# Kernel tuning notes

Hardware: AMD Instinct MI355X
Metric: run time of the kernel (lower is better)

The kernel has to match this reference:

```python
import jax, jax.numpy as jnp
import numpy as np

N, E = 100000, 1200000
IN_DIM, HID, OUT = 128, 64, 64
EPS = 1e-5


def _glorot(key, shape):
    lim = 1.0 / np.sqrt(shape[0])
    return jax.random.uniform(key, shape, jnp.float32, -lim, lim)


def setup_inputs() -> dict:
    key = jax.random.key(0)
    ks = jax.random.split(key, 20)
    inp = {
        'x': jax.random.normal(ks[0], (N, IN_DIM), jnp.float32),
        'edge_index': jax.random.randint(ks[1], (2, E), 0, N, jnp.int64),
        'xgb_scores': jax.random.uniform(ks[2], (N,), jnp.float32),
        # SAGEConv params: W_l (aggregated path, with bias), W_r (root path, no bias)
        'W1l': _glorot(ks[3], (IN_DIM, HID)), 'b1': jnp.zeros((HID,), jnp.float32), 'W1r': _glorot(ks[4], (IN_DIM, HID)),
        'g1': jnp.ones((HID,), jnp.float32), 'be1': jnp.zeros((HID,), jnp.float32),
        'W2l': _glorot(ks[5], (HID, HID)), 'b2': jnp.zeros((HID,), jnp.float32), 'W2r': _glorot(ks[6], (HID, HID)),
        'g2': jnp.ones((HID,), jnp.float32), 'be2': jnp.zeros((HID,), jnp.float32),
        'W3l': _glorot(ks[7], (HID, OUT)), 'b3': jnp.zeros((OUT,), jnp.float32), 'W3r': _glorot(ks[8], (HID, OUT)),
        'g3': jnp.ones((OUT,), jnp.float32), 'be3': jnp.zeros((OUT,), jnp.float32),
        # fusion MLP: Linear(out+1, 64) -> ReLU -> Linear(64, 1)
        'Wf1': _glorot(ks[9], (OUT + 1, 64)), 'bf1': jnp.zeros((64,), jnp.float32),
        'Wf2': _glorot(ks[10], (64, 1)), 'bf2': jnp.zeros((1,), jnp.float32),
    }
    return inp


def _sage_conv(x, src, dst, Wl, b, Wr, n):
    # mean aggregation of source features at destination nodes (PyG SAGEConv, aggr='mean')
    agg = jax.ops.segment_sum(x[src], dst, num_segments=n)           # (N, d)
    cnt = jax.ops.segment_sum(jnp.ones((src.shape[0],), x.dtype), dst, num_segments=n)
    mean = agg / jnp.clip(cnt, 1.0)[:, None]
    return mean @ Wl + b + x @ Wr


def _bn(h, g, b):
    mu = jnp.mean(h, axis=0)
    var = jnp.var(h, axis=0)  # biased, as in torch BN training normalization
    return (h - mu) * jax.lax.rsqrt(var + EPS) * g + b


def reference(x, edge_index, xgb_scores,
              W1l, b1, W1r, g1, be1,
              W2l, b2, W2r, g2, be2,
              W3l, b3, W3r, g3, be3,
              Wf1, bf1, Wf2, bf2):
    n = x.shape[0]
    src, dst = edge_index[0], edge_index[1]
    # dropout is identity in eval; BN uses batch statistics
    h = jax.nn.relu(_bn(_sage_conv(x, src, dst, W1l, b1, W1r, n), g1, be1))
    h = jax.nn.relu(_bn(_sage_conv(h, src, dst, W2l, b2, W2r, n), g2, be2))
    h = jax.nn.relu(_bn(_sage_conv(h, src, dst, W3l, b3, W3r, n), g3, be3))
    combined = jnp.concatenate([h, xgb_scores[:, None]], axis=1)     # (N, out+1)
    z = jax.nn.relu(combined @ Wf1 + bf1)
    logits = (z @ Wf2 + bf2)[:, 0]
    return logits
```

## Files before the change

### kernel.cpp

```cpp
#include <hip/hip_runtime.h>


typedef __attribute__((ext_vector_type(8))) short bf16x8;
typedef __attribute__((ext_vector_type(4))) float f32x4;

#define ELLS 48

__device__ __forceinline__ ushort f2bf(float f) {
  unsigned u = __float_as_uint(f);
  return (ushort)((u + 0x7fff + ((u >> 16) & 1)) >> 16);
}
__device__ __forceinline__ float bf2f(ushort h) {
  return __uint_as_float((unsigned)h << 16);
}
__device__ __forceinline__ void unpack8(uint4 v, float* f) {
  f[0] = __uint_as_float(v.x << 16);
  f[1] = __uint_as_float(v.x & 0xffff0000u);
  f[2] = __uint_as_float(v.y << 16);
  f[3] = __uint_as_float(v.y & 0xffff0000u);
  f[4] = __uint_as_float(v.z << 16);
  f[5] = __uint_as_float(v.z & 0xffff0000u);
  f[6] = __uint_as_float(v.w << 16);
  f[7] = __uint_as_float(v.w & 0xffff0000u);
}


__device__ __forceinline__ void prep_one(const float* __restrict__ Wl,
                                         const float* __restrict__ Wr,
                                         ushort* __restrict__ Whi,
                                         ushort* __restrict__ Wlo, int din,
                                         int i) {
  int col = i / din, k = i % din;
  float v = (col < 64) ? Wl[(size_t)k * 64 + col]
                       : Wr[(size_t)k * 64 + (col - 64)];
  ushort h = f2bf(v);
  Whi[i] = h;
  Wlo[i] = f2bf(v - bf2f(h));
}

__global__ __launch_bounds__(256) void prep_all(
    const float* __restrict__ W1l, const float* __restrict__ W1r,
    ushort* __restrict__ Whi1, ushort* __restrict__ Wlo1,
    const float* __restrict__ W2l, const float* __restrict__ W2r,
    ushort* __restrict__ Whi2, ushort* __restrict__ Wlo2,
    const float* __restrict__ W3l, const float* __restrict__ W3r,
    ushort* __restrict__ Whi3, ushort* __restrict__ Wlo3,
    int* __restrict__ deg, float* __restrict__ stats,
    ushort* __restrict__ sent, int n, int nbd) {
  int bid = blockIdx.x;
  const int tid = threadIdx.x;
  if (bid < nbd) {
    int i = bid * 256 + tid;
    if (i < n + 4) deg[i] = 0;
    return;
  }
  bid -= nbd;
  if (bid < 64) {
    prep_one(W1l, W1r, Whi1, Wlo1, 128, bid * 256 + tid);
    return;
  }
  bid -= 64;
  if (bid < 32) {
    prep_one(W2l, W2r, Whi2, Wlo2, 64, bid * 256 + tid);
    return;
  }
  bid -= 32;
  if (bid < 32) {
    prep_one(W3l, W3r, Whi3, Wlo3, 64, bid * 256 + tid);
    return;
  }
  if (tid < 384) stats[tid] = 0.f;
  if (tid < 64) sent[tid] = 0;
}


__global__ __launch_bounds__(256) void ell_fill_sharded(
    const int* __restrict__ ei, int* __restrict__ deg, int* __restrict__ ell,
    int E, int n, int bps) {
  const int shard = blockIdx.x / bps;
  const int bib = blockIdx.x % bps;
  const int chunk = n >> 3;
  const int lo = shard * chunk;
  const int hi = (shard == 7) ? n : lo + chunk;
  for (int e = bib * 256 + threadIdx.x; e < E; e += bps * 256) {
    int d = __builtin_nontemporal_load(ei + E + e);
    if (d >= lo && d < hi) {
      int s = __builtin_nontemporal_load(ei + e);
      int pos = atomicAdd(&deg[d], 1);
      if (pos < ELLS) ell[(size_t)d * ELLS + pos] = s;
    }
  }
}

template <int DIN, bool NORM, bool XBF16>
__global__ __launch_bounds__(256) void gemm_mfma(
    const void* __restrict__ Xv, const float* __restrict__ stats,
    const float* __restrict__ g, const float* __restrict__ be,
    const float* __restrict__ bias, const ushort* __restrict__ Whi,
    const ushort* __restrict__ Wlo, ushort* __restrict__ Ybf,
    ushort* __restrict__ Yrbf, int n) {
  constexpr int WS = 40;
  __shared__ ushort sW[2 * 128 * WS];
  __shared__ float sSS[128];
  __shared__ float sB[64];
  const int tid = threadIdx.x;
  const int w = tid >> 6;
  const int lane = tid & 63;
  const int m = lane & 15;
  const int quad = lane >> 4;
  const int row0 = blockIdx.x * 64;

  if (tid < 64) {
    sB[tid] = bias[tid];
    if (NORM) {
      float invn = 1.0f / (float)n;
      float mu = stats[tid] * invn;
      float var = fmaf(-mu, mu, stats[64 + tid] * invn);
      float sc = g[tid] * rsqrtf(var + 1e-5f);
      sSS[tid] = sc;
      sSS[64 + tid] = fmaf(-mu, sc, be[tid]);
    }
  }

  const int arow = min(row0 + w * 16 + m, n - 1);

  f32x4 acc[8];
#pragma unroll
  for (int t = 0; t < 8; t++) acc[t] = (f32x4){0.f, 0.f, 0.f, 0.f};

  for (int kc = 0; kc < DIN; kc += 32) {
    __syncthreads();
    for (int i = tid; i < 512; i += 256) {
      int col = i >> 2;
      int k = (i & 3) * 8;
      *reinterpret_cast<uint4*>(sW + col * WS + k) =
          *reinterpret_cast<const uint4*>(Whi + (size_t)col * DIN + kc + k);
      *reinterpret_cast<uint4*>(sW + 128 * WS + col * WS + k) =
          *reinterpret_cast<const uint4*>(Wlo + (size_t)col * DIN + kc + k);
    }
    __syncthreads();

    const int kb = kc + quad * 8;
    float av[8];
    if (XBF16) {
      const ushort* X = (const ushort*)Xv;
      uint4 v = *reinterpret_cast<const uint4*>(X + (size_t)arow * DIN + kb);
      unpack8(v, av);
    } else {
      const float* X = (const float*)Xv;
      const float* ap = X + (size_t)arow * DIN + kb;
      float4 a0 = *reinterpret_cast<const float4*>(ap);
      float4 a1 = *reinterpret_cast<const float4*>(ap + 4);
      av[0] = a0.x; av[1] = a0.y; av[2] = a0.z; av[3] = a0.w;
      av[4] = a1.x; av[5] = a1.y; av[6] = a1.z; av[7] = a1.w;
    }
    if (NORM) {
#pragma unroll
      for (int j = 0; j < 8; j++)
        av[j] = fmaxf(fmaf(av[j], sSS[kb + j], sSS[64 + kb + j]), 0.f);
    }
    bf16x8 Ahi, Alo;
#pragma unroll
    for (int j = 0; j < 8; j++) {
      ushort h = f2bf(av[j]);
      Ahi[j] = (short)h;
      Alo[j] = (short)f2bf(av[j] - bf2f(h));
    }
#pragma unroll
    for (int t = 0; t < 8; t++) {
      bf16x8 Bhi =
          *reinterpret_cast<const bf16x8*>(sW + (t * 16 + m) * WS + quad * 8);
      bf16x8 Blo = *reinterpret_cast<const bf16x8*>(sW + 128 * WS +
                                                    (t * 16 + m) * WS +
                                                    quad * 8);
      acc[t] = __builtin_amdgcn_mfma_f32_16x16x32_bf16(Ahi, Bhi, acc[t], 0, 0, 0);
      acc[t] = __builtin_amdgcn_mfma_f32_16x16x32_bf16(Ahi, Blo, acc[t], 0, 0, 0);
      acc[t] = __builtin_amdgcn_mfma_f32_16x16x32_bf16(Alo, Bhi, acc[t], 0, 0, 0);
    }
  }

#pragma unroll
  for (int t = 0; t < 8; t++) {
    int col = t * 16 + m;
#pragma unroll
    for (int r = 0; r < 4; r++) {
      int grow = row0 + w * 16 + quad * 4 + r;
      if (grow < n) {
        float v = acc[t][r];
        if (t < 4) {
          Ybf[(size_t)grow * 64 + col] = f2bf(v);
        } else {
          Yrbf[(size_t)grow * 64 + (col - 64)] = f2bf(v + sB[col - 64]);
        }
      }
    }
  }
}

__global__ __launch_bounds__(256) void gather_combine(
    const ushort* __restrict__ Ybf, const ushort* __restrict__ Yrbf,
    const int* __restrict__ ell, const int* __restrict__ deg,
    ushort* __restrict__ Tbf, float* __restrict__ stats, int n) {
  const int lane = threadIdx.x & 63;
  const int w = threadIdx.x >> 6;
  const int grp = lane >> 3;
  const int sub = lane & 7;
  const int wid = blockIdx.x * 4 + w;
  const int nw = gridDim.x * 4;
  float ssum[8], ssq[8];
#pragma unroll
  for (int c = 0; c < 8; c++) ssum[c] = ssq[c] = 0.f;

  for (int base = wid * 4; base < n; base += nw * 4) {
    int4 dg4 = *reinterpret_cast<const int4*>(deg + base);
    int dg[4] = {dg4.x, dg4.y, dg4.z, dg4.w};
    int mx = 0;
#pragma unroll
    for (int j = 0; j < 4; j++) mx = max(mx, min(dg[j], ELLS));
    float a[4][8];
#pragma unroll
    for (int j = 0; j < 4; j++)
#pragma unroll
      for (int c = 0; c < 8; c++) a[j][c] = 0.f;

    for (int e0 = 0; e0 < mx; e0 += 8) {
      int idx = e0 + grp;
      int s0 = ell[(size_t)(base + 0) * ELLS + idx];
      int s1 = ell[(size_t)(base + 1) * ELLS + idx];
      int s2 = ell[(size_t)(base + 2) * ELLS + idx];
      int s3 = ell[(size_t)(base + 3) * ELLS + idx];
      s0 = (idx < dg[0]) ? s0 : n;
      s1 = (idx < dg[1]) ? s1 : n;
      s2 = (idx < dg[2]) ? s2 : n;
      s3 = (idx < dg[3]) ? s3 : n;
      uint4 v0 = *reinterpret_cast<const uint4*>(Ybf + (size_t)s0 * 64 + sub * 8);
      uint4 v1 = *reinterpret_cast<const uint4*>(Ybf + (size_t)s1 * 64 + sub * 8);
      uint4 v2 = *reinterpret_cast<const uint4*>(Ybf + (size_t)s2 * 64 + sub * 8);
      uint4 v3 = *reinterpret_cast<const uint4*>(Ybf + (size_t)s3 * 64 + sub * 8);
      float f[8];
      unpack8(v0, f);
#pragma unroll
      for (int c = 0; c < 8; c++) a[0][c] += f[c];
      unpack8(v1, f);
#pragma unroll
      for (int c = 0; c < 8; c++) a[1][c] += f[c];
      unpack8(v2, f);
#pragma unroll
      for (int c = 0; c < 8; c++) a[2][c] += f[c];
      unpack8(v3, f);
#pragma unroll
      for (int c = 0; c < 8; c++) a[3][c] += f[c];
    }
#pragma unroll
    for (int mmask = 8; mmask <= 32; mmask <<= 1)
#pragma unroll
      for (int j = 0; j < 4; j++)
#pragma unroll
        for (int c = 0; c < 8; c++)
          a[j][c] += __shfl_xor(a[j][c], mmask, 64);

    if (lane < 8) {
#pragma unroll
      for (int j = 0; j < 4; j++) {
        int node = base + j;
        if (node >= n) continue;
        float iv = 1.0f / (float)max(dg[j], 1);
        uint4 yrv =
            *reinterpret_cast<const uint4*>(Yrbf + (size_t)node * 64 + sub * 8);
        float yr[8];
        unpack8(yrv, yr);
        float t[8];
#pragma unroll
        for (int c = 0; c < 8; c++) {
          t[c] = fmaf(a[j][c], iv, yr[c]);
          ssum[c] += t[c];
          ssq[c] = fmaf(t[c], t[c], ssq[c]);
        }
        uint4 o;
        o.x = (uint)f2bf(t[0]) | ((uint)f2bf(t[1]) << 16);
        o.y = (uint)f2bf(t[2]) | ((uint)f2bf(t[3]) << 16);
        o.z = (uint)f2bf(t[4]) | ((uint)f2bf(t[5]) << 16);
        o.w = (uint)f2bf(t[6]) | ((uint)f2bf(t[7]) << 16);
        *reinterpret_cast<uint4*>(Tbf + (size_t)node * 64 + sub * 8) = o;
      }
    }
  }
  __shared__ float rS[4][64];
  __shared__ float rQ[4][64];
  if (lane < 8) {
#pragma unroll
    for (int c = 0; c < 8; c++) {
      rS[w][sub * 8 + c] = ssum[c];
      rQ[w][sub * 8 + c] = ssq[c];
    }
  }
  __syncthreads();
  if (threadIdx.x < 64) {
    int tc = threadIdx.x;
    float s = rS[0][tc] + rS[1][tc] + rS[2][tc] + rS[3][tc];
    float qq = rQ[0][tc] + rQ[1][tc] + rQ[2][tc] + rQ[3][tc];
    atomicAdd(&stats[tc], s);
    atomicAdd(&stats[64 + tc], qq);
  }
}


__global__ __launch_bounds__(256) void fusion_fused(
    const ushort* __restrict__ Tbf, const float* __restrict__ stats,
    const float* __restrict__ g, const float* __restrict__ be,
    const float* __restrict__ xgb, const float* __restrict__ Wf1,
    const float* __restrict__ bf1, const float* __restrict__ Wf2,
    const float* __restrict__ bf2, float* __restrict__ out, int n) {
  __shared__ float sH[64 * 64];
  __shared__ float sW1[65 * 64];
  __shared__ float sW2[64];
  __shared__ float sSS[128];
  const int tid = threadIdx.x;
  const int c = tid & 63;
  const int w = tid >> 6;
  const int row0 = blockIdx.x * 64;
  if (tid < 64) {
    float invn = 1.0f / (float)n;
    float mu = stats[tid] * invn;
    float var = fmaf(-mu, mu, stats[64 + tid] * invn);
    float sc = g[tid] * rsqrtf(var + 1e-5f);
    sSS[tid] = sc;
    sSS[64 + tid] = fmaf(-mu, sc, be[tid]);
  }
  for (int i = tid; i < 65 * 64; i += 256) sW1[i] = Wf1[i];
  if (tid < 64) sW2[tid] = Wf2[tid];
  __syncthreads();
  for (int i = tid; i < 512; i += 256) {
    int r = i >> 3;
    int k = (i & 7) * 8;
    int row = min(row0 + r, n - 1);
    uint4 v = *reinterpret_cast<const uint4*>(Tbf + (size_t)row * 64 + k);
    float f[8];
    unpack8(v, f);
#pragma unroll
    for (int j = 0; j < 8; j++)
      f[j] = fmaxf(fmaf(f[j], sSS[k + j], sSS[64 + k + j]), 0.f);
    *reinterpret_cast<float4*>(sH + r * 64 + k) =
        make_float4(f[0], f[1], f[2], f[3]);
    *reinterpret_cast<float4*>(sH + r * 64 + k + 4) =
        make_float4(f[4], f[5], f[6], f[7]);
  }
  __syncthreads();
  const float b1v = bf1[c];
  const float wx = sW1[64 * 64 + c];
  const float w2v = sW2[c];
  const float b2v = bf2[0];
  float acc[16];
#pragma unroll
  for (int r = 0; r < 16; r++) acc[r] = b1v;
  for (int kk = 0; kk < 64; kk += 4) {
    float4 hv[16];
#pragma unroll
    for (int r = 0; r < 16; r++)
      hv[r] = *reinterpret_cast<const float4*>(sH + (w * 16 + r) * 64 + kk);
    float w0 = sW1[(kk + 0) * 64 + c];
    float w1 = sW1[(kk + 1) * 64 + c];
    float w2 = sW1[(kk + 2) * 64 + c];
    float w3 = sW1[(kk + 3) * 64 + c];
#pragma unroll
    for (int r = 0; r < 16; r++) {
      acc[r] = fmaf(hv[r].x, w0, acc[r]);
      acc[r] = fmaf(hv[r].y, w1, acc[r]);
      acc[r] = fmaf(hv[r].z, w2, acc[r]);
      acc[r] = fmaf(hv[r].w, w3, acc[r]);
    }
  }
#pragma unroll
  for (int r = 0; r < 16; r++) {
    int row = row0 + w * 16 + r;
    float xv = (row < n) ? xgb[row] : 0.f;
    float z = fmaxf(fmaf(xv, wx, acc[r]), 0.f) * w2v;
#pragma unroll
    for (int off = 32; off > 0; off >>= 1) z += __shfl_xor(z, off, 64);
    if (row < n && c == 0) out[row] = z + b2v;
  }
}


extern "C" void kernel_launch(void* const* d_in, const int* in_sizes, int n_in,
                              void* d_out, int out_size, void* d_ws,
                              size_t ws_size, hipStream_t stream) {
  const float* x = (const float*)d_in[0];
  const int* ei = (const int*)d_in[1];
  const float* xgb = (const float*)d_in[2];
  const float* W1l = (const float*)d_in[3];
  const float* b1 = (const float*)d_in[4];
  const float* W1r = (const float*)d_in[5];
  const float* g1 = (const float*)d_in[6];
  const float* be1 = (const float*)d_in[7];
  const float* W2l = (const float*)d_in[8];
  const float* b2 = (const float*)d_in[9];
  const float* W2r = (const float*)d_in[10];
  const float* g2 = (const float*)d_in[11];
  const float* be2 = (const float*)d_in[12];
  const float* W3l = (const float*)d_in[13];
  const float* b3 = (const float*)d_in[14];
  const float* W3r = (const float*)d_in[15];
  const float* g3 = (const float*)d_in[16];
  const float* be3 = (const float*)d_in[17];
  const float* Wf1 = (const float*)d_in[18];
  const float* bf1 = (const float*)d_in[19];
  const float* Wf2 = (const float*)d_in[20];
  const float* bf2 = (const float*)d_in[21];
  float* out = (float*)d_out;

  const int n = in_sizes[2];
  const int E = in_sizes[1] / 2;

  char* w = (char*)d_ws;
  auto alloc = [&](size_t bytes) {
    void* p = (void*)w;
    w += (bytes + 255) & ~(size_t)255;
    return p;
  };
  int* deg = (int*)alloc((size_t)(n + 4) * 4);
  int* ell = (int*)alloc((size_t)(n + 4) * ELLS * 4);
  ushort* Ybf = (ushort*)alloc((size_t)(n + 1) * 64 * 2);
  ushort* Yrbf = (ushort*)alloc((size_t)n * 64 * 2);
  ushort* Tbf = (ushort*)alloc((size_t)n * 64 * 2);
  ushort* Whi1 = (ushort*)alloc(128 * 128 * 2);
  ushort* Wlo1 = (ushort*)alloc(128 * 128 * 2);
  ushort* Whi2 = (ushort*)alloc(128 * 64 * 2);
  ushort* Wlo2 = (ushort*)alloc(128 * 64 * 2);
  ushort* Whi3 = (ushort*)alloc(128 * 64 * 2);
  ushort* Wlo3 = (ushort*)alloc(128 * 64 * 2);
  float* stats = (float*)alloc(3 * 128 * 4);

  const int nbd = (n + 4 + 255) / 256;
  prep_all<<<nbd + 64 + 32 + 32 + 1, 256, 0, stream>>>(
      W1l, W1r, Whi1, Wlo1, W2l, W2r, Whi2, Wlo2, W3l, W3r, Whi3, Wlo3, deg,
      stats, Ybf + (size_t)n * 64, n, nbd);

  const int bps = 2048;
  ell_fill_sharded<<<8 * bps, 256, 0, stream>>>(ei, deg, ell, E, n, bps);

  const int gTile = (n + 63) / 64;
  const int gGath = 2048;

  gemm_mfma<128, false, false><<<gTile, 256, 0, stream>>>(
      x, nullptr, nullptr, nullptr, b1, Whi1, Wlo1, Ybf, Yrbf, n);
  gather_combine<<<gGath, 256, 0, stream>>>(Ybf, Yrbf, ell, deg, Tbf,
                                            stats + 0, n);

  gemm_mfma<64, true, true><<<gTile, 256, 0, stream>>>(
      Tbf, stats + 0, g1, be1, b2, Whi2, Wlo2, Ybf, Yrbf, n);
  gather_combine<<<gGath, 256, 0, stream>>>(Ybf, Yrbf, ell, deg, Tbf,
                                            stats + 128, n);

  gemm_mfma<64, true, true><<<gTile, 256, 0, stream>>>(
      Tbf, stats + 128, g2, be2, b3, Whi3, Wlo3, Ybf, Yrbf, n);
  gather_combine<<<gGath, 256, 0, stream>>>(Ybf, Yrbf, ell, deg, Tbf,
                                            stats + 256, n);

  fusion_fused<<<gTile, 256, 0, stream>>>(Tbf, stats + 256, g3, be3, xgb, Wf1,
                                          bf1, Wf2, bf2, out, n);
}
```

Before: 480.2 us.

## Stage GEMM outputs through LDS, read fusion weights from global, shrink ELL fill grid

The GEMM epilogue now writes bf16 results into shared memory, reusing the weight buffer, and then emits full 16-byte coalesced row stores to Ybf/Yrbf. Before, each lane issued scattered 2-byte stores. The fusion kernel drops its shared-memory copy of Wf1/Wf2 and reads them straight from global/L1, which cuts LDS use and staging time. The ELL fill grid shrinks from 2048 to 512 blocks per shard. The costs are two extra barriers in the GEMM and uncached-style global weight loads inside the fusion inner loop.

Result: no change. 489.7 us (+2.0%).

```diff
diff --git a/kernel.cpp b/kernel.cpp
--- a/kernel.cpp
+++ b/kernel.cpp
@@ -179,19 +179,30 @@
     }
   }
 
+  __syncthreads();
+  ushort* sY = sW;
 #pragma unroll
   for (int t = 0; t < 8; t++) {
     int col = t * 16 + m;
+    float badd = (t >= 4) ? sB[col - 64] : 0.f;
 #pragma unroll
     for (int r = 0; r < 4; r++) {
-      int grow = row0 + w * 16 + quad * 4 + r;
-      if (grow < n) {
-        float v = acc[t][r];
-        if (t < 4) {
-          Ybf[(size_t)grow * 64 + col] = f2bf(v);
-        } else {
-          Yrbf[(size_t)grow * 64 + (col - 64)] = f2bf(v + sB[col - 64]);
-        }
+      sY[(w * 16 + quad * 4 + r) * 136 + col] = f2bf(acc[t][r] + badd);
+    }
+  }
+  __syncthreads();
+  {
+    const int row = tid >> 2;
+    const int seg = tid & 3;
+    const int grow = row0 + row;
+    if (grow < n) {
+      const ushort* src = sY + row * 136 + seg * 32;
+      ushort* dstp = (seg < 2) ? (Ybf + (size_t)grow * 64 + seg * 32)
+                               : (Yrbf + (size_t)grow * 64 + (seg - 2) * 32);
+#pragma unroll
+      for (int j = 0; j < 4; j++) {
+        *reinterpret_cast<uint4*>(dstp + j * 8) =
+            *reinterpret_cast<const uint4*>(src + j * 8);
       }
     }
   }
@@ -312,8 +323,6 @@
     const float* __restrict__ bf1, const float* __restrict__ Wf2,
     const float* __restrict__ bf2, float* __restrict__ out, int n) {
   __shared__ float sH[64 * 64];
-  __shared__ float sW1[65 * 64];
-  __shared__ float sW2[64];
   __shared__ float sSS[128];
   const int tid = threadIdx.x;
   const int c = tid & 63;
@@ -327,8 +336,6 @@
     sSS[tid] = sc;
     sSS[64 + tid] = fmaf(-mu, sc, be[tid]);
   }
-  for (int i = tid; i < 65 * 64; i += 256) sW1[i] = Wf1[i];
-  if (tid < 64) sW2[tid] = Wf2[tid];
   __syncthreads();
   for (int i = tid; i < 512; i += 256) {
     int r = i >> 3;
@@ -347,8 +354,8 @@
   }
   __syncthreads();
   const float b1v = bf1[c];
-  const float wx = sW1[64 * 64 + c];
-  const float w2v = sW2[c];
+  const float wx = Wf1[64 * 64 + c];
+  const float w2v = Wf2[c];
   const float b2v = bf2[0];
   float acc[16];
 #pragma unroll
@@ -358,10 +365,10 @@
 #pragma unroll
     for (int r = 0; r < 16; r++)
       hv[r] = *reinterpret_cast<const float4*>(sH + (w * 16 + r) * 64 + kk);
-    float w0 = sW1[(kk + 0) * 64 + c];
-    float w1 = sW1[(kk + 1) * 64 + c];
-    float w2 = sW1[(kk + 2) * 64 + c];
-    float w3 = sW1[(kk + 3) * 64 + c];
+    float w0 = Wf1[(kk + 0) * 64 + c];
+    float w1 = Wf1[(kk + 1) * 64 + c];
+    float w2 = Wf1[(kk + 2) * 64 + c];
+    float w3 = Wf1[(kk + 3) * 64 + c];
 #pragma unroll
     for (int r = 0; r < 16; r++) {
       acc[r] = fmaf(hv[r].x, w0, acc[r]);
@@ -436,7 +443,7 @@
       W1l, W1r, Whi1, Wlo1, W2l, W2r, Whi2, Wlo2, W3l, W3r, Whi3, Wlo3, deg,
       stats, Ybf + (size_t)n * 64, n, nbd);
 
-  const int bps = 2048;
+  const int bps = 512;
   ell_fill_sharded<<<8 * bps, 256, 0, stream>>>(ei, deg, ell, E, n, bps);
 
   const int gTile = (n + 63) / 64;
```
